# Performance work log

Measured on AMD Instinct MI355X. Metric: run time of the kernel, lower is better.

Reference implementation:

```python
import jax, jax.numpy as jnp
import numpy as np

B, Q, K, H = 16, 512, 512, 64
DQ, DK, DV = 256, 256, 256
MASK_VAL = -1000000.0


def setup_inputs() -> dict:
    key = jax.random.key(0)
    ks = jax.random.split(key, 7)
    queries = jax.random.normal(ks[0], (B, Q, DQ), dtype=jnp.float32)
    keys = jax.random.normal(ks[1], (B, K, DK), dtype=jnp.float32)
    values = jax.random.normal(ks[2], (B, K, DV), dtype=jnp.float32)
    valid_lens = jax.random.randint(ks[3], (B,), 1, K + 1).astype(jnp.int32)
    # learned params (nn.Linear, bias=False): weight shape [out, in]
    Wq = jax.random.normal(ks[4], (H, DQ), dtype=jnp.float32) / np.sqrt(DQ)
    Wk = jax.random.normal(ks[5], (H, DK), dtype=jnp.float32) / np.sqrt(DK)
    wv = jax.random.normal(ks[6], (H,), dtype=jnp.float32) / np.sqrt(H)
    return {"queries": queries, "keys": keys, "values": values,
            "valid_lens": valid_lens, "Wq": Wq, "Wk": Wk, "wv": wv}


def reference(queries, keys, values, valid_lens, Wq, Wk, wv):
    q = jnp.einsum('bqd,hd->bqh', queries, Wq)          # [B,Q,H]
    k = jnp.einsum('bkd,hd->bkh', keys, Wk)             # [B,K,H]
    feats = jnp.tanh(q[:, :, None, :] + k[:, None, :, :])  # [B,Q,K,H]
    scores = jnp.einsum('bqkh,h->bqk', feats, wv)       # [B,Q,K]
    kmask = jnp.arange(K)[None, None, :] < valid_lens[:, None, None]
    scores = jnp.where(kmask, scores, MASK_VAL)
    attn = jax.nn.softmax(scores, axis=-1)              # [B,Q,K]
    return jnp.einsum('bqk,bkv->bqv', attn, values)     # [B,Q,DV]
```

## Files before the change

kernel.cpp:

```cpp
#include <hip/hip_runtime.h>
#include <math.h>

#if defined(__has_builtin)
#  if __has_builtin(__builtin_amdgcn_exp2f)
#    define EXP2F(x) __builtin_amdgcn_exp2f(x)
#  endif
#  if __has_builtin(__builtin_amdgcn_rcpf)
#    define RCPF(x) __builtin_amdgcn_rcpf(x)
#  endif
#endif
#ifndef EXP2F
#  define EXP2F(x) exp2f(x)
#endif
#ifndef RCPF
#  define RCPF(x) (1.0f/(x))
#endif

static constexpr int Bn = 16, QN = 512, KN = 512, Hn = 64, DV = 256, DIN = 256;
static constexpr int TQ = 8;
static constexpr float TWO_LOG2E = 2.8853900817779268f;
static constexpr float LOG2E     = 1.4426950408889634f;

typedef __attribute__((ext_vector_type(8))) short short8;
typedef __attribute__((ext_vector_type(4))) float f32x4;

__device__ __forceinline__ short f2bf(float x) {
  unsigned u = __builtin_bit_cast(unsigned, x);
  u += 0x7FFF + ((u >> 16) & 1);
  return (short)(u >> 16);
}
__device__ __forceinline__ float bf2f(short h) {
  return __builtin_bit_cast(float, ((unsigned)(unsigned short)h) << 16);
}

__global__ __launch_bounds__(256) void prep_kernel(
    const float* __restrict__ Wq, const float* __restrict__ Wk,
    ushort* __restrict__ wqh, ushort* __restrict__ wql,
    ushort* __restrict__ wkh, ushort* __restrict__ wkl)
{
  int i = blockIdx.x * 256 + threadIdx.x;
  float xq = Wq[i];
  short hq = f2bf(xq);
  wqh[i] = (ushort)hq; wql[i] = (ushort)f2bf(xq - bf2f(hq));
  float xk = Wk[i];
  short hk = f2bf(xk);
  wkh[i] = (ushort)hk; wkl[i] = (ushort)f2bf(xk - bf2f(hk));
}

__global__ __launch_bounds__(256) void proj_mfma(
    const float* __restrict__ queries, const float* __restrict__ keys,
    const ushort* __restrict__ wqh, const ushort* __restrict__ wql,
    const ushort* __restrict__ wkh, const ushort* __restrict__ wkl,
    float* __restrict__ qe, float* __restrict__ ekT)
{
  __shared__ float tr[4][16][20];
  int t = threadIdx.x;
  int lane = t & 63, wid = t >> 6;
  bool is_k = blockIdx.x >= 512;
  int trow = (blockIdx.x & 511) * 16;
  const float*  X  = is_k ? keys : queries;
  const ushort* Wh = is_k ? wkh : wqh;
  const ushort* Wl = is_k ? wkl : wql;
  int mr = lane & 15, quad = lane >> 4;
  const float*  xp  = X  + (size_t)(trow + mr) * DIN + quad * 8;
  const ushort* whp = Wh + (size_t)(wid * 16 + mr) * DIN + quad * 8;
  const ushort* wlp = Wl + (size_t)(wid * 16 + mr) * DIN + quad * 8;

  f32x4 acc = (f32x4){0.f, 0.f, 0.f, 0.f};
  #pragma unroll
  for (int kc = 0; kc < 8; ++kc) {
    float4 a0 = *(const float4*)(xp + kc * 32);
    float4 a1 = *(const float4*)(xp + kc * 32 + 4);
    float av[8] = {a0.x, a0.y, a0.z, a0.w, a1.x, a1.y, a1.z, a1.w};
    short8 ah, al;
    #pragma unroll
    for (int j = 0; j < 8; ++j) {
      ah[j] = f2bf(av[j]);
      al[j] = f2bf(av[j] - bf2f(ah[j]));
    }
    short8 bh = *(const short8*)(whp + kc * 32);
    short8 bl = *(const short8*)(wlp + kc * 32);
    acc = __builtin_amdgcn_mfma_f32_16x16x32_bf16(al, bh, acc, 0, 0, 0);
    acc = __builtin_amdgcn_mfma_f32_16x16x32_bf16(ah, bl, acc, 0, 0, 0);
    acc = __builtin_amdgcn_mfma_f32_16x16x32_bf16(ah, bh, acc, 0, 0, 0);
  }
  if (!is_k) {
    #pragma unroll
    for (int reg = 0; reg < 4; ++reg) {
      int row = trow + quad * 4 + reg;
      qe[(size_t)row * Hn + wid * 16 + mr] = EXP2F(acc[reg] * TWO_LOG2E);
    }
  } else {
    #pragma unroll
    for (int reg = 0; reg < 4; ++reg)
      tr[wid][mr][quad * 4 + reg] = EXP2F(acc[reg] * TWO_LOG2E);
    int b = trow >> 9, kr = trow & (KN - 1);
    #pragma unroll
    for (int hp = 0; hp < 4; ++hp) {
      int h_l = hp * 4 + quad, k_l = mr;
      ekT[((size_t)b * Hn + wid * 16 + h_l) * KN + kr + k_l] = tr[wid][h_l][k_l];
    }
  }
}

__global__ __launch_bounds__(512) void attn_kernel(
    const float* __restrict__ qe,
    const float* __restrict__ ekT,
    const float* __restrict__ values,
    const int*   __restrict__ valid_lens,
    const float* __restrict__ wv,
    float* __restrict__ out)
{
  __shared__ __align__(16) float qes2[Hn][TQ];
  __shared__ __align__(16) float pt[KN][12];
  __shared__ __align__(16) float pacc[3][TQ][DV];
  __shared__ float wsum[8][TQ];
  __shared__ float inv_s[TQ];

  int t = threadIdx.x;
  int lane = t & 63, wave = t >> 6;

  int iA = blockIdx.x, iB = 1023 - blockIdx.x;
  int rankA = iA >> 6, rankB = iB >> 6;
  int bA = 0, bB = 0;
  for (int bb = 0; bb < Bn; ++bb) {
    int Lb = valid_lens[bb];
    int r = 0;
    for (int b2 = 0; b2 < Bn; ++b2) {
      int L2 = valid_lens[b2];
      r += (L2 > Lb || (L2 == Lb && b2 < bb)) ? 1 : 0;
    }
    if (r == rankA) bA = bb;
    if (r == rankB) bB = bb;
  }
  int tb[2] = {bA, bB};
  int tq[2] = {(iA & 63) * TQ, (iB & 63) * TQ};

  float S = 0.f;
  #pragma unroll
  for (int h = 0; h < Hn; ++h) S += wv[h];

  for (int ti = 0; ti < 2; ++ti) {
    int b = tb[ti], q0 = tq[ti];
    int L = valid_lens[b];

    qes2[t >> 3][t & 7] = qe[(size_t)(b * QN + q0 + (t & 7)) * Hn + (t >> 3)];
    __syncthreads();

    {
      int k = t;
      float p[TQ];
      if (k < L) {
        float sc[TQ];
        #pragma unroll
        for (int r = 0; r < TQ; ++r) sc[r] = S;
        const float* kb = ekT + (size_t)b * Hn * KN + k;
        for (int h0 = 0; h0 < Hn; h0 += 8) {
          float ekv[8];
          #pragma unroll
          for (int j = 0; j < 8; ++j)
            ekv[j] = kb[(size_t)(h0 + j) * KN];
          #pragma unroll
          for (int jp = 0; jp < 4; ++jp) {
            int ha = h0 + 2 * jp;
            float wa = 2.0f * wv[ha], wb = 2.0f * wv[ha + 1];
            float eka = ekv[2 * jp], ekb = ekv[2 * jp + 1];
            float4 qa0 = *(const float4*)&qes2[ha][0];
            float4 qa1 = *(const float4*)&qes2[ha][4];
            float4 qb0 = *(const float4*)&qes2[ha + 1][0];
            float4 qb1 = *(const float4*)&qes2[ha + 1][4];
            {
              float da, db, num;
              da = qa0.x * eka + 1.0f; db = qb0.x * ekb + 1.0f;
              num = wa * db + wb * da; sc[0] -= num * RCPF(da * db);
              da = qa0.y * eka + 1.0f; db = qb0.y * ekb + 1.0f;
              num = wa * db + wb * da; sc[1] -= num * RCPF(da * db);
              da = qa0.z * eka + 1.0f; db = qb0.z * ekb + 1.0f;
              num = wa * db + wb * da; sc[2] -= num * RCPF(da * db);
              da = qa0.w * eka + 1.0f; db = qb0.w * ekb + 1.0f;
              num = wa * db + wb * da; sc[3] -= num * RCPF(da * db);
              da = qa1.x * eka + 1.0f; db = qb1.x * ekb + 1.0f;
              num = wa * db + wb * da; sc[4] -= num * RCPF(da * db);
              da = qa1.y * eka + 1.0f; db = qb1.y * ekb + 1.0f;
              num = wa * db + wb * da; sc[5] -= num * RCPF(da * db);
              da = qa1.z * eka + 1.0f; db = qb1.z * ekb + 1.0f;
              num = wa * db + wb * da; sc[6] -= num * RCPF(da * db);
              da = qa1.w * eka + 1.0f; db = qb1.w * ekb + 1.0f;
              num = wa * db + wb * da; sc[7] -= num * RCPF(da * db);
            }
          }
        }
        #pragma unroll
        for (int r = 0; r < TQ; ++r) p[r] = EXP2F(sc[r] * LOG2E);
        *(float4*)&pt[k][0] = make_float4(p[0], p[1], p[2], p[3]);
        *(float4*)&pt[k][4] = make_float4(p[4], p[5], p[6], p[7]);
      } else {
        #pragma unroll
        for (int r = 0; r < TQ; ++r) p[r] = 0.f;
      }
      #pragma unroll
      for (int r = 0; r < TQ; ++r) {
        float s = p[r];
        #pragma unroll
        for (int off = 32; off > 0; off >>= 1) s += __shfl_xor(s, off, 64);
        if (lane == r) wsum[wave][r] = s;
      }
    }
    __syncthreads();
    if (t < TQ) {
      float s = 0.f;
      #pragma unroll
      for (int w = 0; w < 8; ++w) s += wsum[w][t];
      inv_s[t] = 1.0f / s;
    }

    int cp = t & 127, kq = t >> 7;
    int c = 2 * cp;
    int k0 = (L * kq) >> 2, k1 = (L * (kq + 1)) >> 2;
    float a0[TQ], a1[TQ];
    #pragma unroll
    for (int r = 0; r < TQ; ++r) { a0[r] = 0.f; a1[r] = 0.f; }
    const float* vb = values + (size_t)b * KN * DV + c;
    #pragma unroll 2
    for (int k = k0; k < k1; ++k) {
      float2 v2 = *(const float2*)(vb + (size_t)k * DV);
      float4 pa = *(const float4*)&pt[k][0];
      float4 pb = *(const float4*)&pt[k][4];
      a0[0] += pa.x * v2.x; a1[0] += pa.x * v2.y;
      a0[1] += pa.y * v2.x; a1[1] += pa.y * v2.y;
      a0[2] += pa.z * v2.x; a1[2] += pa.z * v2.y;
      a0[3] += pa.w * v2.x; a1[3] += pa.w * v2.y;
      a0[4] += pb.x * v2.x; a1[4] += pb.x * v2.y;
      a0[5] += pb.y * v2.x; a1[5] += pb.y * v2.y;
      a0[6] += pb.z * v2.x; a1[6] += pb.z * v2.y;
      a0[7] += pb.w * v2.x; a1[7] += pb.w * v2.y;
    }
    if (kq) {
      #pragma unroll
      for (int r = 0; r < TQ; ++r)
        *(float2*)&pacc[kq - 1][r][c] = make_float2(a0[r], a1[r]);
    }
    __syncthreads();
    if (kq == 0) {
      float* ob = out + (size_t)(b * QN + q0) * DV + c;
      #pragma unroll
      for (int r = 0; r < TQ; ++r) {
        float s0 = a0[r], s1 = a1[r];
        #pragma unroll
        for (int q = 0; q < 3; ++q) {
          float2 pp = *(const float2*)&pacc[q][r][c];
          s0 += pp.x; s1 += pp.y;
        }
        float iv = inv_s[r];
        *(float2*)(ob + (size_t)r * DV) = make_float2(s0 * iv, s1 * iv);
      }
    }
    __syncthreads();
  }
}

extern "C" void kernel_launch(void* const* d_in, const int* in_sizes, int n_in,
                              void* d_out, int out_size, void* d_ws, size_t ws_size,
                              hipStream_t stream) {
  const float* queries    = (const float*)d_in[0];
  const float* keys       = (const float*)d_in[1];
  const float* values     = (const float*)d_in[2];
  const int*   valid_lens = (const int*)d_in[3];
  const float* Wq         = (const float*)d_in[4];
  const float* Wk         = (const float*)d_in[5];
  const float* wv         = (const float*)d_in[6];
  float* out = (float*)d_out;

  char* ws = (char*)d_ws;
  float*  qe  = (float*)ws;
  float*  ekT = qe + (size_t)Bn * QN * Hn;
  ushort* wqh = (ushort*)(ekT + (size_t)Bn * Hn * KN);
  ushort* wql = wqh + Hn * DIN;
  ushort* wkh = wql + Hn * DIN;
  ushort* wkl = wkh + Hn * DIN;

  prep_kernel<<<64, 256, 0, stream>>>(Wq, Wk, wqh, wql, wkh, wkl);
  proj_mfma<<<1024, 256, 0, stream>>>(queries, keys, wqh, wql, wkh, wkl, qe, ekT);
  attn_kernel<<<512, 512, 0, stream>>>(qe, ekT, values, valid_lens, wv, out);
}
```

Before: 152.8 us.

## Launch one tile per block with rank-balanced batch mapping across CU slots

Changes the attention launch from 512 blocks that each process two tiles (a long-rank and a short-rank pair) to 1024 blocks that each handle one tile. Batch ranks are assigned per slot in a mirrored and shifted pattern so that each CU's set of blocks mixes long and short valid lengths. The batch sort is now done once in parallel by 16 threads into shared memory. The PV stage changes from 4 k-quarters with 2 columns per thread to 2 k-halves with 1 column per thread, which shrinks the partial-sum buffer. This relies on a block-to-CU dispatch order that the hardware does not guarantee, and it drops the reuse of per-block setup across two tiles.

Result: faster. 149.5 us (-2.2%).

```diff
diff --git a/kernel.cpp b/kernel.cpp
--- a/kernel.cpp
+++ b/kernel.cpp
@@ -113,149 +113,136 @@
 {
   __shared__ __align__(16) float qes2[Hn][TQ];
   __shared__ __align__(16) float pt[KN][12];
-  __shared__ __align__(16) float pacc[3][TQ][DV];
+  __shared__ __align__(16) float pacc[TQ][DV];
   __shared__ float wsum[8][TQ];
   __shared__ float inv_s[TQ];
+  __shared__ int srank[Bn];
 
   int t = threadIdx.x;
   int lane = t & 63, wave = t >> 6;
 
-  int iA = blockIdx.x, iB = 1023 - blockIdx.x;
-  int rankA = iA >> 6, rankB = iB >> 6;
-  int bA = 0, bB = 0;
-  for (int bb = 0; bb < Bn; ++bb) {
-    int Lb = valid_lens[bb];
+  if (t < Bn) {
+    int Lb = valid_lens[t];
     int r = 0;
+    #pragma unroll
     for (int b2 = 0; b2 < Bn; ++b2) {
       int L2 = valid_lens[b2];
-      r += (L2 > Lb || (L2 == Lb && b2 < bb)) ? 1 : 0;
-    }
-    if (r == rankA) bA = bb;
-    if (r == rankB) bB = bb;
-  }
-  int tb[2] = {bA, bB};
-  int tq[2] = {(iA & 63) * TQ, (iB & 63) * TQ};
+      r += (L2 > Lb || (L2 == Lb && b2 < t)) ? 1 : 0;
+    }
+    srank[r] = t;
+  }
+  __syncthreads();
+
+  int cu = blockIdx.x & 255, slot = blockIdx.x >> 8;
+  int m = cu >> 4;
+  int jr = (slot == 0) ? m
+         : (slot == 1) ? 15 - m
+         : (slot == 2) ? ((m + 8) & 15)
+                       : 15 - ((m + 8) & 15);
+  int b = srank[jr];
+  int q0 = (slot * 16 + (cu & 15)) * TQ;
+  int L = valid_lens[b];
+
+  qes2[t >> 3][t & 7] = qe[(size_t)(b * QN + q0 + (t & 7)) * Hn + (t >> 3)];
+  __syncthreads();
 
   float S = 0.f;
   #pragma unroll
   for (int h = 0; h < Hn; ++h) S += wv[h];
 
-  for (int ti = 0; ti < 2; ++ti) {
-    int b = tb[ti], q0 = tq[ti];
-    int L = valid_lens[b];
-
-    qes2[t >> 3][t & 7] = qe[(size_t)(b * QN + q0 + (t & 7)) * Hn + (t >> 3)];
-    __syncthreads();
-
-    {
-      int k = t;
-      float p[TQ];
-      if (k < L) {
-        float sc[TQ];
+  {
+    int k = t;
+    float p[TQ];
+    if (k < L) {
+      float sc[TQ];
+      #pragma unroll
+      for (int r = 0; r < TQ; ++r) sc[r] = S;
+      const float* kb = ekT + (size_t)b * Hn * KN + k;
+      for (int h0 = 0; h0 < Hn; h0 += 8) {
+        float ekv[8];
         #pragma unroll
-        for (int r = 0; r < TQ; ++r) sc[r] = S;
-        const float* kb = ekT + (size_t)b * Hn * KN + k;
-        for (int h0 = 0; h0 < Hn; h0 += 8) {
-          float ekv[8];
-          #pragma unroll
-          for (int j = 0; j < 8; ++j)
-            ekv[j] = kb[(size_t)(h0 + j) * KN];
-          #pragma unroll
-          for (int jp = 0; jp < 4; ++jp) {
-            int ha = h0 + 2 * jp;
-            float wa = 2.0f * wv[ha], wb = 2.0f * wv[ha + 1];
-            float eka = ekv[2 * jp], ekb = ekv[2 * jp + 1];
-            float4 qa0 = *(const float4*)&qes2[ha][0];
-            float4 qa1 = *(const float4*)&qes2[ha][4];
-            float4 qb0 = *(const float4*)&qes2[ha + 1][0];
-            float4 qb1 = *(const float4*)&qes2[ha + 1][4];
-            {
-              float da, db, num;
-              da = qa0.x * eka + 1.0f; db = qb0.x * ekb + 1.0f;
-              num = wa * db + wb * da; sc[0] -= num * RCPF(da * db);
-              da = qa0.y * eka + 1.0f; db = qb0.y * ekb + 1.0f;
-              num = wa * db + wb * da; sc[1] -= num * RCPF(da * db);
-              da = qa0.z * eka + 1.0f; db = qb0.z * ekb + 1.0f;
-              num = wa * db + wb * da; sc[2] -= num * RCPF(da * db);
-              da = qa0.w * eka + 1.0f; db = qb0.w * ekb + 1.0f;
-              num = wa * db + wb * da; sc[3] -= num * RCPF(da * db);
-              da = qa1.x * eka + 1.0f; db = qb1.x * ekb + 1.0f;
-              num = wa * db + wb * da; sc[4] -= num * RCPF(da * db);
-              da = qa1.y * eka + 1.0f; db = qb1.y * ekb + 1.0f;
-              num = wa * db + wb * da; sc[5] -= num * RCPF(da * db);
-              da = qa1.z * eka + 1.0f; db = qb1.z * ekb + 1.0f;
-              num = wa * db + wb * da; sc[6] -= num * RCPF(da * db);
-              da = qa1.w * eka + 1.0f; db = qb1.w * ekb + 1.0f;
-              num = wa * db + wb * da; sc[7] -= num * RCPF(da * db);
-            }
-          }
+        for (int j = 0; j < 8; ++j)
+          ekv[j] = kb[(size_t)(h0 + j) * KN];
+        #pragma unroll
+        for (int jp = 0; jp < 4; ++jp) {
+          int ha = h0 + 2 * jp;
+          float wa = 2.0f * wv[ha], wb = 2.0f * wv[ha + 1];
+          float eka = ekv[2 * jp], ekb = ekv[2 * jp + 1];
+          float4 qa0 = *(const float4*)&qes2[ha][0];
+          float4 qa1 = *(const float4*)&qes2[ha][4];
+          float4 qb0 = *(const float4*)&qes2[ha + 1][0];
+          float4 qb1 = *(const float4*)&qes2[ha + 1][4];
+          float da, db, num;
+          da = qa0.x * eka + 1.0f; db = qb0.x * ekb + 1.0f;
+          num = wa * db + wb * da; sc[0] -= num * RCPF(da * db);
+          da = qa0.y * eka + 1.0f; db = qb0.y * ekb + 1.0f;
+          num = wa * db + wb * da; sc[1] -= num * RCPF(da * db);
+          da = qa0.z * eka + 1.0f; db = qb0.z * ekb + 1.0f;
+          num = wa * db + wb * da; sc[2] -= num * RCPF(da * db);
+          da = qa0.w * eka + 1.0f; db = qb0.w * ekb + 1.0f;
+          num = wa * db + wb * da; sc[3] -= num * RCPF(da * db);
+          da = qa1.x * eka + 1.0f; db = qb1.x * ekb + 1.0f;
+          num = wa * db + wb * da; sc[4] -= num * RCPF(da * db);
+          da = qa1.y * eka + 1.0f; db = qb1.y * ekb + 1.0f;
+          num = wa * db + wb * da; sc[5] -= num * RCPF(da * db);
+          da = qa1.z * eka + 1.0f; db = qb1.z * ekb + 1.0f;
+          num = wa * db + wb * da; sc[6] -= num * RCPF(da * db);
+          da = qa1.w * eka + 1.0f; db = qb1.w * ekb + 1.0f;
+          num = wa * db + wb * da; sc[7] -= num * RCPF(da * db);
         }
-        #pragma unroll
-        for (int r = 0; r < TQ; ++r) p[r] = EXP2F(sc[r] * LOG2E);
-        *(float4*)&pt[k][0] = make_float4(p[0], p[1], p[2], p[3]);
-        *(float4*)&pt[k][4] = make_float4(p[4], p[5], p[6], p[7]);
-      } else {
-        #pragma unroll
-        for (int r = 0; r < TQ; ++r) p[r] = 0.f;
       }
       #pragma unroll
-      for (int r = 0; r < TQ; ++r) {
-        float s = p[r];
-        #pragma unroll
-        for (int off = 32; off > 0; off >>= 1) s += __shfl_xor(s, off, 64);
-        if (lane == r) wsum[wave][r] = s;
-      }
-    }
-    __syncthreads();
-    if (t < TQ) {
-      float s = 0.f;
-      #pragma unroll
-      for (int w = 0; w < 8; ++w) s += wsum[w][t];
-      inv_s[t] = 1.0f / s;
-    }
-
-    int cp = t & 127, kq = t >> 7;
-    int c = 2 * cp;
-    int k0 = (L * kq) >> 2, k1 = (L * (kq + 1)) >> 2;
-    float a0[TQ], a1[TQ];
-    #pragma unroll
-    for (int r = 0; r < TQ; ++r) { a0[r] = 0.f; a1[r] = 0.f; }
-    const float* vb = values + (size_t)b * KN * DV + c;
-    #pragma unroll 2
-    for (int k = k0; k < k1; ++k) {
-      float2 v2 = *(const float2*)(vb + (size_t)k * DV);
-      float4 pa = *(const float4*)&pt[k][0];
-      float4 pb = *(const float4*)&pt[k][4];
-      a0[0] += pa.x * v2.x; a1[0] += pa.x * v2.y;
-      a0[1] += pa.y * v2.x; a1[1] += pa.y * v2.y;
-      a0[2] += pa.z * v2.x; a1[2] += pa.z * v2.y;
-      a0[3] += pa.w * v2.x; a1[3] += pa.w * v2.y;
-      a0[4] += pb.x * v2.x; a1[4] += pb.x * v2.y;
-      a0[5] += pb.y * v2.x; a1[5] += pb.y * v2.y;
-      a0[6] += pb.z * v2.x; a1[6] += pb.z * v2.y;
-      a0[7] += pb.w * v2.x; a1[7] += pb.w * v2.y;
-    }
-    if (kq) {
-      #pragma unroll
-      for (int r = 0; r < TQ; ++r)
-        *(float2*)&pacc[kq - 1][r][c] = make_float2(a0[r], a1[r]);
-    }
-    __syncthreads();
-    if (kq == 0) {
-      float* ob = out + (size_t)(b * QN + q0) * DV + c;
-      #pragma unroll
-      for (int r = 0; r < TQ; ++r) {
-        float s0 = a0[r], s1 = a1[r];
-        #pragma unroll
-        for (int q = 0; q < 3; ++q) {
-          float2 pp = *(const float2*)&pacc[q][r][c];
-          s0 += pp.x; s1 += pp.y;
-        }
-        float iv = inv_s[r];
-        *(float2*)(ob + (size_t)r * DV) = make_float2(s0 * iv, s1 * iv);
-      }
-    }
-    __syncthreads();
+      for (int r = 0; r < TQ; ++r) p[r] = EXP2F(sc[r] * LOG2E);
+      *(float4*)&pt[k][0] = make_float4(p[0], p[1], p[2], p[3]);
+      *(float4*)&pt[k][4] = make_float4(p[4], p[5], p[6], p[7]);
+    } else {
+      #pragma unroll
+      for (int r = 0; r < TQ; ++r) p[r] = 0.f;
+    }
+    #pragma unroll
+    for (int r = 0; r < TQ; ++r) {
+      float s = p[r];
+      #pragma unroll
+      for (int off = 32; off > 0; off >>= 1) s += __shfl_xor(s, off, 64);
+      if (lane == r) wsum[wave][r] = s;
+    }
+  }
+  __syncthreads();
+  if (t < TQ) {
+    float s = 0.f;
+    #pragma unroll
+    for (int w = 0; w < 8; ++w) s += wsum[w][t];
+    inv_s[t] = 1.0f / s;
+  }
+
+  int c = t & (DV - 1), half = t >> 8;
+  int mid = L >> 1;
+  int k0 = half ? mid : 0;
+  int k1 = half ? L : mid;
+  float acc[TQ];
+  #pragma unroll
+  for (int r = 0; r < TQ; ++r) acc[r] = 0.f;
+  const float* vb = values + (size_t)b * KN * DV + c;
+  #pragma unroll 4
+  for (int k = k0; k < k1; ++k) {
+    float val = vb[(size_t)k * DV];
+    float4 pa = *(const float4*)&pt[k][0];
+    float4 pb = *(const float4*)&pt[k][4];
+    acc[0] += pa.x * val; acc[1] += pa.y * val;
+    acc[2] += pa.z * val; acc[3] += pa.w * val;
+    acc[4] += pb.x * val; acc[5] += pb.y * val;
+    acc[6] += pb.z * val; acc[7] += pb.w * val;
+  }
+  if (half) {
+    #pragma unroll
+    for (int r = 0; r < TQ; ++r) pacc[r][c] = acc[r];
+  }
+  __syncthreads();
+  if (!half) {
+    float* ob = out + (size_t)(b * QN + q0) * DV + c;
+    #pragma unroll
+    for (int r = 0; r < TQ; ++r)
+      ob[(size_t)r * DV] = (acc[r] + pacc[r][c]) * inv_s[r];
   }
 }
 
@@ -281,5 +268,6 @@
 
   prep_kernel<<<64, 256, 0, stream>>>(Wq, Wk, wqh, wql, wkh, wkl);
   proj_mfma<<<1024, 256, 0, stream>>>(queries, keys, wqh, wql, wkh, wkl, qe, ekT);
-  attn_kernel<<<512, 512, 0, stream>>>(qe, ekT, values, valid_lens, wv, out);
-}
+  attn_kernel<<<Bn * (QN / TQ), 512, 0, stream>>>(qe, ekT, values,
+                                                  valid_lens, wv, out);
+}
```
